# Optimization experiments

Measured on AMD Instinct MI355X. Metric: run time of the kernel, lower is better.

Reference implementation:

```python
import jax, jax.numpy as jnp
import numpy as np

# dims
B, F, K = 64, 4096, 8
D_IN = D_SLOT = D_KVQ = 192
HID = 768
N_ITERS = 3
EPS = 1e-8
GROUPS = [(0, 1), (1, 7), (7, 8)]  # bg / fg / ag contiguous slot slices
SB_STRENGTH = 1.0
SB_SIGMA = 0.25
GRID = 64  # sqrt(F)


def _layernorm(x, g, b):
    m = jnp.mean(x, axis=-1, keepdims=True)
    v = jnp.mean(jnp.square(x - m), axis=-1, keepdims=True)
    return (x - m) * jax.lax.rsqrt(v + 1e-5) * g + b


def _gru_cell(x, h, Wih, Whh, bih, bhh):
    # torch.nn.GRUCell semantics; gate order r, z, n
    gi = x @ Wih.T + bih
    gh = h @ Whh.T + bhh
    ir, iz, i_n = jnp.split(gi, 3, axis=-1)
    hr, hz, h_n = jnp.split(gh, 3, axis=-1)
    r = jax.nn.sigmoid(ir + hr)
    z = jax.nn.sigmoid(iz + hz)
    n = jnp.tanh(i_n + r * h_n)
    return (1.0 - z) * n + z * h


def _token_coords():
    y = np.linspace(-1.0, 1.0, GRID, dtype=np.float32)
    x = np.linspace(-1.0, 1.0, GRID, dtype=np.float32)
    yy, xx = np.meshgrid(y, x, indexing='ij')
    return jnp.asarray(np.stack((xx, yy), axis=-1).reshape(F, 2))


def setup_inputs() -> dict:
    key = jax.random.key(0)
    ks = jax.random.split(key, 16)
    def n(i, shape, s=0.02):
        return jax.random.normal(ks[i], shape, jnp.float32) * s
    return dict(
        features=jax.random.normal(ks[0], (B, F, D_IN), jnp.float32),
        slots=jax.random.normal(ks[1], (B, K, D_SLOT), jnp.float32),
        Wk=n(2, (D_IN, D_KVQ)), Wv=n(3, (D_IN, D_KVQ)), Wq=n(4, (D_SLOT, D_KVQ)),
        ln_feat_g=jnp.ones(D_IN), ln_feat_b=jnp.zeros(D_IN),
        ln_slot_g=jnp.ones(D_SLOT), ln_slot_b=jnp.zeros(D_SLOT),
        gru_Wih=n(5, (3, 3 * D_SLOT, D_KVQ)), gru_Whh=n(6, (3, 3 * D_SLOT, D_SLOT)),
        gru_bih=n(7, (3, 3 * D_SLOT)), gru_bhh=n(8, (3, 3 * D_SLOT)),
        mlp_ln_g=jnp.ones((3, D_SLOT)), mlp_ln_b=jnp.zeros((3, D_SLOT)),
        mlp_W1=n(9, (3, D_SLOT, HID)), mlp_b1=n(10, (3, HID)),
        mlp_W2=n(11, (3, HID, D_SLOT)), mlp_b2=n(12, (3, D_SLOT)),
    )


def reference(features, slots, Wk, Wv, Wq, ln_feat_g, ln_feat_b, ln_slot_g,
              ln_slot_b, gru_Wih, gru_Whh, gru_bih, gru_bhh, mlp_ln_g,
              mlp_ln_b, mlp_W1, mlp_b1, mlp_W2, mlp_b2):
    coords = _token_coords()  # (F, 2)
    f = _layernorm(features, ln_feat_g, ln_feat_b)
    k = f @ Wk  # (B, F, Dk)
    v = f @ Wv
    scale = D_KVQ ** -0.5
    sigma2 = max(SB_SIGMA ** 2, 1e-8)
    prev_attn = None
    for _ in range(N_ITERS):
        slots_prev = slots
        q = _layernorm(slots, ln_slot_g, ln_slot_b) @ Wq  # (B, K, Dk)
        dots = jnp.einsum('bkd,bfd->bkf', q, k) * scale
        if prev_attn is not None and SB_STRENGTH > 0.0:
            w = prev_attn / (prev_attn.sum(-1, keepdims=True) + 1e-8)
            centers = jnp.einsum('bkf,fd->bkd', w, coords)  # (B, K, 2)
            diff = coords[None, None] - centers[:, :, None]  # (B, K, F, 2)
            dist2 = jnp.sum(diff * diff, axis=-1)
            dots = dots + SB_STRENGTH * (-dist2 / (2.0 * sigma2))
        attn = jax.nn.softmax(dots, axis=1)  # competition over slots
        prev_attn = attn
        w = attn / (attn.sum(-1, keepdims=True) + EPS)  # weighted mean over F
        updates = jnp.einsum('bkf,bfd->bkd', w, v)  # (B, K, Dk)
        outs = []
        for g, (s, e) in enumerate(GROUPS):
            u = updates[:, s:e].reshape(-1, D_KVQ)
            h_prev = slots_prev[:, s:e].reshape(-1, D_SLOT)
            h = _gru_cell(u, h_prev, gru_Wih[g], gru_Whh[g], gru_bih[g], gru_bhh[g])
            x = _layernorm(h, mlp_ln_g[g], mlp_ln_b[g])
            x = jax.nn.relu(x @ mlp_W1[g] + mlp_b1[g]) @ mlp_W2[g] + mlp_b2[g]
            outs.append((h + x).reshape(B, e - s, D_SLOT))
        slots = jnp.concatenate(outs, axis=1)
    return slots
```

## Files before the change

kernel.cpp:

```cpp
#include <hip/hip_runtime.h>

typedef unsigned short u16;
typedef unsigned int u32;

#define BB 64
#define FF 4096
#define DD 192
#define HH 768

typedef __attribute__((ext_vector_type(8))) __bf16 bf16x8;
typedef __attribute__((ext_vector_type(4))) float f32x4;

__device__ __forceinline__ float bf2f(u32 u) {
  union { u32 i; float f; } x; x.i = u << 16; return x.f;
}
__device__ __forceinline__ u16 f2bf(float f) {
  __bf16 h = (__bf16)f;
  return __builtin_bit_cast(u16, h);
}
__device__ __forceinline__ u32 pk2bf(float a, float b) {
  return (u32)f2bf(a) | ((u32)f2bf(b) << 16);
}
__device__ __forceinline__ float sigm(float x) { return 1.f / (1.f + __expf(-x)); }

__global__ void prep_wmod(const float* __restrict__ Wk, const float* __restrict__ Wv,
                          const float* __restrict__ g, const float* __restrict__ bb,
                          u16* __restrict__ wmodT, float* __restrict__ s1,
                          float* __restrict__ s0) {
  int n = blockIdx.x * 64 + threadIdx.x;
  const float* W = (n < DD) ? Wk : Wv;
  int col = (n < DD) ? n : n - DD;
  float a1 = 0.f, a0 = 0.f;
  for (int e = 0; e < DD; ++e) {
    float w = W[e * DD + col];
    u16 h = f2bf(g[e] * w);
    wmodT[n * DD + e] = h;
    a1 += bf2f(h);
    a0 += bb[e] * w;
  }
  s1[n] = a1; s0[n] = a0;
}

__global__ void prep_packw(const float* __restrict__ Wih, const float* __restrict__ Whh,
                           const float* __restrict__ W1, const float* __restrict__ W2,
                           u16* __restrict__ pWih, u16* __restrict__ pWhh,
                           u16* __restrict__ pW1, u16* __restrict__ pW2) {
  int which = blockIdx.y;
  int total, N, E;
  const float* src; u16* dst; int srcEmajor;
  if (which < 2) { total = 3 * 576 * 192; N = 576; E = 192; srcEmajor = 0;
                   src = which ? Whh : Wih; dst = which ? pWhh : pWih; }
  else if (which == 2) { total = 3 * 192 * 768; N = 768; E = 192; srcEmajor = 1;
                         src = W1; dst = pW1; }
  else { total = 3 * 768 * 192; N = 192; E = 768; srcEmajor = 1; src = W2; dst = pW2; }
  for (int idx = blockIdx.x * 256 + threadIdx.x; idx < total; idx += gridDim.x * 256) {
    int g = idx / (N * E), rem = idx % (N * E);
    int n, e;
    if (srcEmajor) { e = rem / N; n = rem % N; }
    else { n = rem / E; e = rem % E; }
    dst[((g * (E / 2) + (e >> 1)) * N + n) * 2 + (e & 1)] = f2bf(src[idx]);
  }
}

__global__ __launch_bounds__(256, 4) void proj_kernel(
    const float* __restrict__ feat, const u16* __restrict__ wmodT,
    const float* __restrict__ s1, const float* __restrict__ s0,
    u16* __restrict__ kc_, u16* __restrict__ vc_) {
  __shared__ __align__(16) u16 Atile[32 * 192];
  __shared__ float stats[32 * 2];
  int tid = threadIdx.x;
  long tile_base = (long)blockIdx.x * 32;
  int w = tid >> 6, lane = tid & 63;
  {
    int r = w * 8 + (lane >> 3);
    int p = lane & 7;
    const float4* src = (const float4*)(feat + (tile_base + r) * DD) + p * 6;
    float s = 0.f, s2 = 0.f;
    #pragma unroll
    for (int i = 0; i < 6; ++i) {
      float4 v = src[i];
      s += v.x + v.y + v.z + v.w;
      s2 += v.x * v.x + v.y * v.y + v.z * v.z + v.w * v.w;
      uint2 pk;
      pk.x = pk2bf(v.x, v.y);
      pk.y = pk2bf(v.z, v.w);
      int u = p * 3 + (i >> 1);
      *(uint2*)((char*)Atile + r * 384 + ((u ^ (r & 7)) << 4) + (i & 1) * 8) = pk;
    }
    s += __shfl_xor(s, 1); s2 += __shfl_xor(s2, 1);
    s += __shfl_xor(s, 2); s2 += __shfl_xor(s2, 2);
    s += __shfl_xor(s, 4); s2 += __shfl_xor(s2, 4);
    if (p == 0) {
      float mu = s * (1.f / 192.f);
      stats[r * 2] = mu;
      stats[r * 2 + 1] = rsqrtf(s2 * (1.f / 192.f) - mu * mu + 1e-5f);
    }
  }
  __syncthreads();
  int l15 = lane & 15, l4 = lane >> 4;
  f32x4 acc[2][6];
  #pragma unroll
  for (int a = 0; a < 2; ++a)
    #pragma unroll
    for (int b2 = 0; b2 < 6; ++b2) acc[a][b2] = (f32x4){0.f, 0.f, 0.f, 0.f};
  #pragma unroll
  for (int kk = 0; kk < 6; ++kk) {
    bf16x8 afr[2];
    #pragma unroll
    for (int mt = 0; mt < 2; ++mt) {
      int row = mt * 16 + l15;
      int u = kk * 4 + l4;
      afr[mt] = *(bf16x8*)((char*)Atile + row * 384 + ((u ^ (row & 7)) << 4));
    }
    bf16x8 bfr[6];
    #pragma unroll
    for (int nt = 0; nt < 6; ++nt) {
      int col = w * 96 + nt * 16 + l15;
      bfr[nt] = *(const bf16x8*)(wmodT + col * DD + kk * 32 + l4 * 8);
    }
    #pragma unroll
    for (int mt = 0; mt < 2; ++mt)
      #pragma unroll
      for (int nt = 0; nt < 6; ++nt)
        acc[mt][nt] = __builtin_amdgcn_mfma_f32_16x16x32_bf16(afr[mt], bfr[nt],
                                                              acc[mt][nt], 0, 0, 0);
  }
  __syncthreads();
  long bidx = tile_base / FF;
  int f0 = (int)(tile_base % FF);
  if (w < 2) {
    #pragma unroll
    for (int nt = 0; nt < 6; ++nt) {
      int col = w * 96 + nt * 16 + l15;
      float s1c = s1[col], s0c = s0[col];
      int u = col >> 3, ce = (col & 7) * 2;
      #pragma unroll
      for (int mt = 0; mt < 2; ++mt) {
        #pragma unroll
        for (int j = 0; j < 4; ++j) {
          int row = mt * 16 + l4 * 4 + j;
          float mu = stats[row * 2], rstd = stats[row * 2 + 1];
          u16 hv = f2bf(rstd * (acc[mt][nt][j] - mu * s1c) + s0c);
          *(u16*)((char*)Atile + row * 384 + ((u ^ (row & 7)) << 4) + ce) = hv;
        }
      }
    }
  } else {
    #pragma unroll
    for (int nt = 0; nt < 6; ++nt) {
      int col = (w - 2) * 96 + nt * 16 + l15;
      float s1c = s1[col + 192], s0c = s0[col + 192];
      int ntg = col >> 4;
      #pragma unroll
      for (int mt = 0; mt < 2; ++mt) {
        int tl = mt * 16 + l4 * 4;
        int r0 = tl, r1 = tl + 1, r2 = tl + 2, r3 = tl + 3;
        uint2 pk;
        pk.x = pk2bf(stats[r0 * 2 + 1] * (acc[mt][nt][0] - stats[r0 * 2] * s1c) + s0c,
                     stats[r1 * 2 + 1] * (acc[mt][nt][1] - stats[r1 * 2] * s1c) + s0c);
        pk.y = pk2bf(stats[r2 * 2 + 1] * (acc[mt][nt][2] - stats[r2 * 2] * s1c) + s0c,
                     stats[r3 * 2 + 1] * (acc[mt][nt][3] - stats[r3 * 2] * s1c) + s0c);
        u32 ox = __shfl_xor((int)pk.x, 16);
        u32 oy = __shfl_xor((int)pk.y, 16);
        if ((l4 & 1) == 0) {
          int t0 = f0 + tl;
          int g32 = t0 >> 5;
          int l4f = (t0 >> 3) & 3;
          uint4 val = {pk.x, pk.y, ox, oy};
          *(uint4*)(vc_ + ((((long)bidx * 128 + g32) * 12 + ntg) * 64 + l4f * 16 +
                           (col & 15)) * 8) = val;
        }
      }
    }
  }
  __syncthreads();
  {
    long Tg0 = tile_base >> 4;
    #pragma unroll
    for (int p2 = 0; p2 < 3; ++p2) {
      int fi = tid + p2 * 256;
      int tau = fi & 15, u = (fi >> 4) % 24, tt = fi / 384;
      uint4 val = *(uint4*)((char*)Atile + (tt * 16 + tau) * 384 + ((u ^ (tau & 7)) << 4));
      *(uint4*)(kc_ + (((Tg0 + tt) * 24 + u) * 16 + tau) * 8) = val;
    }
  }
}

__global__ __launch_bounds__(64) void qproj_kernel(
    const float* __restrict__ slots, const float* __restrict__ Wq,
    const float* __restrict__ g, const float* __restrict__ bb,
    float* __restrict__ qbuf) {
  __shared__ float ln[192];
  int bk = blockIdx.x;
  int lane = threadIdx.x;
  const float* x = slots + bk * DD;
  float v0 = x[lane], v1 = x[lane + 64], v2 = x[lane + 128];
  float s = v0 + v1 + v2, s2 = v0 * v0 + v1 * v1 + v2 * v2;
  #pragma unroll
  for (int m = 1; m < 64; m <<= 1) { s += __shfl_xor(s, m); s2 += __shfl_xor(s2, m); }
  float mu = s * (1.f / 192.f);
  float rstd = rsqrtf(s2 * (1.f / 192.f) - mu * mu + 1e-5f);
  ln[lane]       = (v0 - mu) * rstd * g[lane]       + bb[lane];
  ln[lane + 64]  = (v1 - mu) * rstd * g[lane + 64]  + bb[lane + 64];
  ln[lane + 128] = (v2 - mu) * rstd * g[lane + 128] + bb[lane + 128];
  __syncthreads();
  float a0 = 0.f, a1 = 0.f, a2 = 0.f;
  for (int e = 0; e < DD; ++e) {
    float le = ln[e];
    a0 += le * Wq[e * DD + lane];
    a1 += le * Wq[e * DD + lane + 64];
    a2 += le * Wq[e * DD + lane + 128];
  }
  const float scale = 0.07216878364870323f;
  qbuf[bk * DD + lane]       = a0 * scale;
  qbuf[bk * DD + lane + 64]  = a1 * scale;
  qbuf[bk * DD + lane + 128] = a2 * scale;
}

__global__ __launch_bounds__(256) void attnupd_kernel(
    const u16* __restrict__ kc_, const u16* __restrict__ vc_,
    const float* __restrict__ qbuf,
    const float* __restrict__ asum_prev, const float* __restrict__ cacc_prev,
    float* __restrict__ upd, float* __restrict__ asum_cur,
    float* __restrict__ cacc_cur, int have_bias) {
  __shared__ __align__(16) u16 qlds[16 * 192];
  __shared__ __align__(16) u16 attn_lds[16 * 256];
  int b = blockIdx.x;
  int chunk = blockIdx.y * 256;
  int tid = threadIdx.x;
  if (tid < 192) {
    int s = tid / 24, u = tid % 24;
    const float* qp = qbuf + (b * 8 + s) * DD + u * 8;
    uint4 p;
    p.x = pk2bf(qp[0], qp[1]);
    p.y = pk2bf(qp[2], qp[3]);
    p.z = pk2bf(qp[4], qp[5]);
    p.w = pk2bf(qp[6], qp[7]);
    *(uint4*)((char*)qlds + s * 384 + ((u ^ (s & 7)) << 4)) = p;
  } else {
    int t2 = tid - 192;
    #pragma unroll
    for (int i = 0; i < 3; ++i) {
      int idx = t2 * 3 + i;
      int s = 8 + idx / 24, u = idx % 24;
      *(uint4*)((char*)qlds + s * 384 + ((u ^ (s & 7)) << 4)) = (uint4){0, 0, 0, 0};
    }
    #pragma unroll
    for (int i = 0; i < 4; ++i)
      *(uint4*)((char*)attn_lds + 4096 + (t2 * 4 + i) * 16) = (uint4){0, 0, 0, 0};
  }
  __syncthreads();
  int w = tid >> 6, lane = tid & 63;
  int l15 = lane & 15, l4 = lane >> 4;
  bf16x8 qfr[6];
  #pragma unroll
  for (int kk = 0; kk < 6; ++kk) {
    int u = kk * 4 + l4;
    qfr[kk] = *(bf16x8*)((char*)qlds + l15 * 384 + ((u ^ (l15 & 7)) << 4));
  }
  float ax[4], ay[4], c0[4];
  #pragma unroll
  for (int j = 0; j < 4; ++j) {
    int s = l4 * 4 + j;
    if (have_bias && s < 8) {
      float inv = 1.f / (asum_prev[b * 8 + s] + 1e-8f);
      float cx = cacc_prev[(b * 8 + s) * 2] * inv;
      float cy = cacc_prev[(b * 8 + s) * 2 + 1] * inv;
      ax[j] = 16.f * cx; ay[j] = 16.f * cy; c0[j] = -8.f * (cx * cx + cy * cy);
    } else { ax[j] = 0.f; ay[j] = 0.f; c0[j] = 0.f; }
  }
  float pa[4], px[4], py[4];
  #pragma unroll
  for (int j = 0; j < 4; ++j) { pa[j] = 0.f; px[j] = 0.f; py[j] = 0.f; }
  for (int tile = w; tile < 16; tile += 4) {
    int t0 = chunk + tile * 16;
    long Tg = (long)b * 256 + (t0 >> 4);
    const u16* kp = kc_ + (Tg * 24 + l4) * 128 + l15 * 8;
    f32x4 acc = (f32x4){0.f, 0.f, 0.f, 0.f};
    #pragma unroll
    for (int kk = 0; kk < 6; ++kk) {
      bf16x8 bfr = *(const bf16x8*)(kp + kk * 512);
      acc = __builtin_amdgcn_mfma_f32_16x16x32_bf16(qfr[kk], bfr, acc, 0, 0, 0);
    }
    int t = t0 + l15;
    float x = -1.f + (float)(t & 63) * (2.f / 63.f);
    float y = -1.f + (float)(t >> 6) * (2.f / 63.f);
    float m8r2 = -8.f * (x * x + y * y);
    float d4[4];
    #pragma unroll
    for (int j = 0; j < 4; ++j)
      d4[j] = acc[j] + (have_bias ? (ax[j] * x + ay[j] * y + c0[j] + m8r2) : 0.f);
    float o4[4];
    #pragma unroll
    for (int j = 0; j < 4; ++j) o4[j] = __shfl_xor(d4[j], 16);
    float mx = fmaxf(fmaxf(fmaxf(d4[0], d4[1]), fmaxf(d4[2], d4[3])),
                     fmaxf(fmaxf(o4[0], o4[1]), fmaxf(o4[2], o4[3])));
    float e4[4];
    float sum = 0.f;
    #pragma unroll
    for (int j = 0; j < 4; ++j) { e4[j] = __expf(d4[j] - mx); sum += e4[j]; }
    #pragma unroll
    for (int j = 0; j < 4; ++j) sum += __expf(o4[j] - mx);
    float inv = 1.f / sum;
    if (l4 < 2) {
      int tl = tile * 16 + l15;
      #pragma unroll
      for (int j = 0; j < 4; ++j) {
        float a = e4[j] * inv;
        int s = l4 * 4 + j;
        *(u16*)((char*)attn_lds + ((s * 512 + tl * 2) ^ ((s & 7) << 4))) = f2bf(a);
        pa[j] += a; px[j] += a * x; py[j] += a * y;
      }
    }
  }
  #pragma unroll
  for (int m = 1; m < 16; m <<= 1) {
    #pragma unroll
    for (int j = 0; j < 4; ++j) {
      pa[j] += __shfl_xor(pa[j], m);
      px[j] += __shfl_xor(px[j], m);
      py[j] += __shfl_xor(py[j], m);
    }
  }
  if (l15 == 0 && l4 < 2) {
    #pragma unroll
    for (int j = 0; j < 4; ++j) {
      int s = l4 * 4 + j;
      atomicAdd(&asum_cur[b * 8 + s], pa[j]);
      atomicAdd(&cacc_cur[(b * 8 + s) * 2], px[j]);
      atomicAdd(&cacc_cur[(b * 8 + s) * 2 + 1], py[j]);
    }
  }
  __syncthreads();
  int g32base = chunk >> 5;
  #pragma unroll
  for (int ni = 0; ni < 3; ++ni) {
    int nt = w * 3 + ni;
    f32x4 acc = (f32x4){0.f, 0.f, 0.f, 0.f};
    const u16* vp = vc_ + ((((long)b * 128 + g32base) * 12 + nt) * 64 + l4 * 16 + l15) * 8;
    #pragma unroll
    for (int gl = 0; gl < 8; ++gl) {
      int tl0 = gl * 32 + l4 * 8;
      bf16x8 afr = *(bf16x8*)((char*)attn_lds + ((l15 * 512 + tl0 * 2) ^ ((l15 & 7) << 4)));
      bf16x8 bfr = *(const bf16x8*)(vp + gl * 12 * 64 * 8);
      acc = __builtin_amdgcn_mfma_f32_16x16x32_bf16(afr, bfr, acc, 0, 0, 0);
    }
    if (l4 < 2) {
      #pragma unroll
      for (int j = 0; j < 4; ++j) {
        int s = l4 * 4 + j;
        atomicAdd(&upd[((long)b * 8 + s) * DD + nt * 16 + l15], acc[j]);
      }
    }
  }
}

template <int M>
__device__ void gru_body(int b0, int g, int srow,
                         float* u_l, float* h_l, float* gi_l, float* gh_l,
                         float* hn_l, float* ln_l, float* x1_l, float* out_l, float* st,
                         const float* __restrict__ upd, const float* __restrict__ asum,
                         const float* __restrict__ sin_,
                         const u16* __restrict__ pWih, const u16* __restrict__ pWhh,
                         const float* __restrict__ bih, const float* __restrict__ bhh,
                         const float* __restrict__ mlng, const float* __restrict__ mlnb,
                         const u16* __restrict__ pW1, const float* __restrict__ b1,
                         const u16* __restrict__ pW2, const float* __restrict__ b2,
                         float* __restrict__ sout) {
  int tid = threadIdx.x;
  for (int idx = tid; idx < M * 192; idx += 768) {
    int row = idx / 192, d = idx % 192;
    int gr = b0 * 8 + srow + row;
    float inv = 1.f / (asum[gr] + 1e-8f);
    u_l[row * 192 + d] = upd[gr * DD + d] * inv;
    h_l[row * 192 + d] = sin_[gr * DD + d];
  }
  __syncthreads();
  if (tid < 576) {
    int c = tid;
    const u16* wih = pWih + (size_t)g * 96 * 1152 + c * 2;
    const u16* whh = pWhh + (size_t)g * 96 * 1152 + c * 2;
    float ai[M], ah[M];
    #pragma unroll
    for (int r = 0; r < M; ++r) { ai[r] = 0.f; ah[r] = 0.f; }
    #pragma unroll 4
    for (int e2 = 0; e2 < 96; ++e2) {
      u32 wi = *(const u32*)(wih + e2 * 1152);
      u32 wh = *(const u32*)(whh + e2 * 1152);
      float wi0 = bf2f(wi & 0xffffu), wi1 = bf2f(wi >> 16);
      float wh0 = bf2f(wh & 0xffffu), wh1 = bf2f(wh >> 16);
      #pragma unroll
      for (int r = 0; r < M; ++r) {
        ai[r] += wi0 * u_l[r * 192 + e2 * 2] + wi1 * u_l[r * 192 + e2 * 2 + 1];
        ah[r] += wh0 * h_l[r * 192 + e2 * 2] + wh1 * h_l[r * 192 + e2 * 2 + 1];
      }
    }
    #pragma unroll
    for (int r = 0; r < M; ++r) { gi_l[r * 576 + c] = ai[r]; gh_l[r * 576 + c] = ah[r]; }
  }
  __syncthreads();
  if (tid < M * 192) {
    int row = tid / 192, uu = tid % 192;
    const float* bihg = bih + g * 576;
    const float* bhhg = bhh + g * 576;
    float r_ = sigm(gi_l[row * 576 + uu] + bihg[uu] + gh_l[row * 576 + uu] + bhhg[uu]);
    float z_ = sigm(gi_l[row * 576 + 192 + uu] + bihg[192 + uu] +
                    gh_l[row * 576 + 192 + uu] + bhhg[192 + uu]);
    float nn = gi_l[row * 576 + 384 + uu] + bihg[384 + uu] +
               r_ * (gh_l[row * 576 + 384 + uu] + bhhg[384 + uu]);
    float t = 1.f - 2.f / (__expf(2.f * nn) + 1.f);
    hn_l[row * 192 + uu] = (1.f - z_) * t + z_ * h_l[row * 192 + uu];
  }
  __syncthreads();
  {
    int wv = tid >> 6, lane = tid & 63;
    if (wv < M) {
      float v0 = hn_l[wv * 192 + lane], v1 = hn_l[wv * 192 + lane + 64],
            v2 = hn_l[wv * 192 + lane + 128];
      float s = v0 + v1 + v2, sq = v0 * v0 + v1 * v1 + v2 * v2;
      #pragma unroll
      for (int m = 1; m < 64; m <<= 1) { s += __shfl_xor(s, m); sq += __shfl_xor(sq, m); }
      if (lane == 0) {
        float mu = s * (1.f / 192.f);
        st[wv * 2] = mu;
        st[wv * 2 + 1] = rsqrtf(sq * (1.f / 192.f) - mu * mu + 1e-5f);
      }
    }
  }
  __syncthreads();
  if (tid < M * 192) {
    int row = tid / 192, uu = tid % 192;
    ln_l[row * 192 + uu] = (hn_l[row * 192 + uu] - st[row * 2]) * st[row * 2 + 1] *
                               mlng[g * DD + uu] + mlnb[g * DD + uu];
  }
  __syncthreads();
  {
    int c = tid;
    const u16* w1 = pW1 + (size_t)g * 96 * 1536 + c * 2;
    float a[M];
    #pragma unroll
    for (int r = 0; r < M; ++r) a[r] = 0.f;
    #pragma unroll 4
    for (int e2 = 0; e2 < 96; ++e2) {
      u32 wp = *(const u32*)(w1 + e2 * 1536);
      float w0 = bf2f(wp & 0xffffu), w1f = bf2f(wp >> 16);
      #pragma unroll
      for (int r = 0; r < M; ++r)
        a[r] += w0 * ln_l[r * 192 + e2 * 2] + w1f * ln_l[r * 192 + e2 * 2 + 1];
    }
    float bc = b1[g * HH + c];
    #pragma unroll
    for (int r = 0; r < M; ++r) x1_l[r * 768 + c] = fmaxf(a[r] + bc, 0.f);
  }
  if (tid < M * 192) {
    int row = tid / 192, uu = tid % 192;
    out_l[row * 192 + uu] = hn_l[row * 192 + uu] + b2[g * DD + uu];
  }
  __syncthreads();
  {
    int c = tid % 192, ks = tid / 192;
    const u16* w2 = pW2 + (size_t)g * 384 * 384 + c * 2;
    float a[M];
    #pragma unroll
    for (int r = 0; r < M; ++r) a[r] = 0.f;
    #pragma unroll 4
    for (int e2 = ks * 96; e2 < ks * 96 + 96; ++e2) {
      u32 wp = *(const u32*)(w2 + e2 * 384);
      float w0 = bf2f(wp & 0xffffu), w1f = bf2f(wp >> 16);
      #pragma unroll
      for (int r = 0; r < M; ++r)
        a[r] += w0 * x1_l[r * 768 + e2 * 2] + w1f * x1_l[r * 768 + e2 * 2 + 1];
    }
    #pragma unroll
    for (int r = 0; r < M; ++r) atomicAdd(&out_l[r * 192 + c], a[r]);
  }
  __syncthreads();
  if (tid < M * 192) {
    int row = tid / 192, d = tid % 192;
    sout[(b0 * 8 + srow + row) * DD + d] = out_l[row * 192 + d];
  }
}

__global__ __launch_bounds__(768) void gru_kernel(
    const float* __restrict__ upd, const float* __restrict__ asum,
    const float* __restrict__ sin_,
    const u16* __restrict__ pWih, const u16* __restrict__ pWhh,
    const float* __restrict__ bih, const float* __restrict__ bhh,
    const float* __restrict__ mlng, const float* __restrict__ mlnb,
    const u16* __restrict__ pW1, const float* __restrict__ b1,
    const u16* __restrict__ pW2, const float* __restrict__ b2,
    float* __restrict__ sout) {
  __shared__ float u_l[3 * 192], h_l[3 * 192], gi_l[3 * 576], gh_l[3 * 576];
  __shared__ float hn_l[3 * 192], ln_l[3 * 192], x1_l[3 * 768], out_l[3 * 192], st[8];
  int b = blockIdx.x, y = blockIdx.y;
  if (y == 0)
    gru_body<1>(b, 0, 0, u_l, h_l, gi_l, gh_l, hn_l, ln_l, x1_l, out_l, st,
                upd, asum, sin_, pWih, pWhh, bih, bhh, mlng, mlnb, pW1, b1, pW2, b2, sout);
  else if (y == 1)
    gru_body<1>(b, 2, 7, u_l, h_l, gi_l, gh_l, hn_l, ln_l, x1_l, out_l, st,
                upd, asum, sin_, pWih, pWhh, bih, bhh, mlng, mlnb, pW1, b1, pW2, b2, sout);
  else if (y == 2)
    gru_body<3>(b, 1, 1, u_l, h_l, gi_l, gh_l, hn_l, ln_l, x1_l, out_l, st,
                upd, asum, sin_, pWih, pWhh, bih, bhh, mlng, mlnb, pW1, b1, pW2, b2, sout);
  else
    gru_body<3>(b, 1, 4, u_l, h_l, gi_l, gh_l, hn_l, ln_l, x1_l, out_l, st,
                upd, asum, sin_, pWih, pWhh, bih, bhh, mlng, mlnb, pW1, b1, pW2, b2, sout);
}

extern "C" void kernel_launch(void* const* d_in, const int* in_sizes, int n_in,
                              void* d_out, int out_size, void* d_ws, size_t ws_size,
                              hipStream_t stream) {
  const float* feat = (const float*)d_in[0];
  const float* slots = (const float*)d_in[1];
  const float* Wk = (const float*)d_in[2];
  const float* Wv = (const float*)d_in[3];
  const float* Wq = (const float*)d_in[4];
  const float* lfg = (const float*)d_in[5];
  const float* lfb = (const float*)d_in[6];
  const float* lsg = (const float*)d_in[7];
  const float* lsb = (const float*)d_in[8];
  const float* gWih = (const float*)d_in[9];
  const float* gWhh = (const float*)d_in[10];
  const float* gbih = (const float*)d_in[11];
  const float* gbhh = (const float*)d_in[12];
  const float* mlng = (const float*)d_in[13];
  const float* mlnb = (const float*)d_in[14];
  const float* W1 = (const float*)d_in[15];
  const float* b1 = (const float*)d_in[16];
  const float* W2 = (const float*)d_in[17];
  const float* b2 = (const float*)d_in[18];
  float* out = (float*)d_out;

  char* ws = (char*)d_ws;
  size_t off = 0;
  auto alloc = [&](size_t bytes) {
    void* p = ws + off;
    off += (bytes + 255) & ~(size_t)255;
    return p;
  };
  u16* kc_    = (u16*)alloc((size_t)BB * FF * DD * 2);
  u16* vc_    = (u16*)alloc((size_t)BB * DD * FF * 2);
  float* qbuf = (float*)alloc((size_t)BB * 8 * DD * 4);
  float* upd  = (float*)alloc((size_t)BB * 8 * DD * 4);
  float* slA  = (float*)alloc((size_t)BB * 8 * DD * 4);
  float* slB  = (float*)alloc((size_t)BB * 8 * DD * 4);
  float* asum0 = (float*)alloc(BB * 8 * 4);
  float* asum1 = (float*)alloc(BB * 8 * 4);
  float* cacc0 = (float*)alloc(BB * 8 * 2 * 4);
  float* cacc1 = (float*)alloc(BB * 8 * 2 * 4);
  u16* wmodT  = (u16*)alloc(384 * DD * 2);
  float* s1   = (float*)alloc(384 * 4);
  float* s0   = (float*)alloc(384 * 4);
  u16* pWih   = (u16*)alloc((size_t)3 * 576 * DD * 2);
  u16* pWhh   = (u16*)alloc((size_t)3 * 576 * DD * 2);
  u16* pW1    = (u16*)alloc((size_t)3 * DD * HH * 2);
  u16* pW2    = (u16*)alloc((size_t)3 * HH * DD * 2);

  prep_wmod<<<6, 64, 0, stream>>>(Wk, Wv, lfg, lfb, wmodT, s1, s0);
  prep_packw<<<dim3(432, 4), 256, 0, stream>>>(gWih, gWhh, W1, W2, pWih, pWhh, pW1, pW2);
  proj_kernel<<<BB * FF / 32, 256, 0, stream>>>(feat, wmodT, s1, s0, kc_, vc_);

  const float* sin_ = slots;
  float* souts[3] = {slA, slB, out};
  float* asums[2] = {asum0, asum1};
  float* caccs[2] = {cacc0, cacc1};
  for (int it = 0; it < 3; ++it) {
    int cur = it & 1, prev = cur ^ 1;
    hipMemsetAsync(upd, 0, BB * 8 * DD * 4, stream);
    hipMemsetAsync(asums[cur], 0, BB * 8 * 4, stream);
    hipMemsetAsync(caccs[cur], 0, BB * 8 * 2 * 4, stream);
    qproj_kernel<<<BB * 8, 64, 0, stream>>>(sin_, Wq, lsg, lsb, qbuf);
    attnupd_kernel<<<dim3(BB, 16), 256, 0, stream>>>(kc_, vc_, qbuf, asums[prev],
                                                     caccs[prev], upd, asums[cur],
                                                     caccs[cur], it > 0 ? 1 : 0);
    gru_kernel<<<dim3(BB, 4), 768, 0, stream>>>(upd, asums[cur], sin_, pWih, pWhh,
                                                gbih, gbhh, mlng, mlnb, pW1, b1, pW2, b2,
                                                souts[it]);
    sin_ = souts[it];
  }
}
```

Before: 490.4 us.

## Restructure projection to per-wave 16-token tiles and fold memsets into qproj

The projection kernel now gives each wave its own 16-token tile. Each wave loads features straight into registers as MFMA A-fragments and computes the LayerNorm stats with shuffles, which removes the shared A-tile staging and block-wide barriers. Each wave loops over the four 96-column output groups and stages K output through a private LDS buffer, so the grid is half as many blocks holding twice the tokens. The three hipMemsetAsync calls per iteration are folded into the qproj kernel, which saves launches. The trade-off is that each wave re-reads the full weight matrix from global/L2, and the 4-group loop is serialized.

```diff
diff --git a/kernel.cpp b/kernel.cpp
--- a/kernel.cpp
+++ b/kernel.cpp
@@ -64,106 +64,97 @@
 
 __global__ __launch_bounds__(256, 4) void proj_kernel(
     const float* __restrict__ feat, const u16* __restrict__ wmodT,
-    const float* __restrict__ s1, const float* __restrict__ s0,
+    const float* __restrict__ s1v, const float* __restrict__ s0v,
     u16* __restrict__ kc_, u16* __restrict__ vc_) {
-  __shared__ __align__(16) u16 Atile[32 * 192];
-  __shared__ float stats[32 * 2];
+  __shared__ __align__(16) u16 Ctile[4][2176];
   int tid = threadIdx.x;
-  long tile_base = (long)blockIdx.x * 32;
   int w = tid >> 6, lane = tid & 63;
-  {
-    int r = w * 8 + (lane >> 3);
-    int p = lane & 7;
-    const float4* src = (const float4*)(feat + (tile_base + r) * DD) + p * 6;
-    float s = 0.f, s2 = 0.f;
-    #pragma unroll
-    for (int i = 0; i < 6; ++i) {
-      float4 v = src[i];
-      s += v.x + v.y + v.z + v.w;
-      s2 += v.x * v.x + v.y * v.y + v.z * v.z + v.w * v.w;
-      uint2 pk;
-      pk.x = pk2bf(v.x, v.y);
-      pk.y = pk2bf(v.z, v.w);
-      int u = p * 3 + (i >> 1);
-      *(uint2*)((char*)Atile + r * 384 + ((u ^ (r & 7)) << 4) + (i & 1) * 8) = pk;
-    }
-    s += __shfl_xor(s, 1); s2 += __shfl_xor(s2, 1);
-    s += __shfl_xor(s, 2); s2 += __shfl_xor(s2, 2);
-    s += __shfl_xor(s, 4); s2 += __shfl_xor(s2, 4);
-    if (p == 0) {
-      float mu = s * (1.f / 192.f);
-      stats[r * 2] = mu;
-      stats[r * 2 + 1] = rsqrtf(s2 * (1.f / 192.f) - mu * mu + 1e-5f);
-    }
-  }
-  __syncthreads();
   int l15 = lane & 15, l4 = lane >> 4;
-  f32x4 acc[2][6];
-  #pragma unroll
-  for (int a = 0; a < 2; ++a)
-    #pragma unroll
-    for (int b2 = 0; b2 < 6; ++b2) acc[a][b2] = (f32x4){0.f, 0.f, 0.f, 0.f};
+  long wtile = (long)blockIdx.x * 4 + w;
+  long tok0 = wtile * 16;
+  int bidx = (int)(wtile >> 8);
+  int f0 = ((int)wtile & 255) * 16;
+  char* ct = (char*)&Ctile[w][0];
+
+  const float* fp = feat + (tok0 + l15) * DD + l4 * 8;
+  float4 xa[6], xb[6];
   #pragma unroll
   for (int kk = 0; kk < 6; ++kk) {
-    bf16x8 afr[2];
-    #pragma unroll
-    for (int mt = 0; mt < 2; ++mt) {
-      int row = mt * 16 + l15;
-      int u = kk * 4 + l4;
-      afr[mt] = *(bf16x8*)((char*)Atile + row * 384 + ((u ^ (row & 7)) << 4));
-    }
-    bf16x8 bfr[6];
-    #pragma unroll
-    for (int nt = 0; nt < 6; ++nt) {
-      int col = w * 96 + nt * 16 + l15;
-      bfr[nt] = *(const bf16x8*)(wmodT + col * DD + kk * 32 + l4 * 8);
-    }
-    #pragma unroll
-    for (int mt = 0; mt < 2; ++mt)
-      #pragma unroll
-      for (int nt = 0; nt < 6; ++nt)
-        acc[mt][nt] = __builtin_amdgcn_mfma_f32_16x16x32_bf16(afr[mt], bfr[nt],
-                                                              acc[mt][nt], 0, 0, 0);
-  }
-  __syncthreads();
-  long bidx = tile_base / FF;
-  int f0 = (int)(tile_base % FF);
-  if (w < 2) {
-    #pragma unroll
-    for (int nt = 0; nt < 6; ++nt) {
-      int col = w * 96 + nt * 16 + l15;
-      float s1c = s1[col], s0c = s0[col];
-      int u = col >> 3, ce = (col & 7) * 2;
-      #pragma unroll
-      for (int mt = 0; mt < 2; ++mt) {
+    xa[kk] = *(const float4*)(fp + kk * 32);
+    xb[kk] = *(const float4*)(fp + kk * 32 + 4);
+  }
+  float s = 0.f, s2 = 0.f;
+  bf16x8 afr[6];
+  #pragma unroll
+  for (int kk = 0; kk < 6; ++kk) {
+    float4 a = xa[kk], b = xb[kk];
+    s += a.x + a.y + a.z + a.w + b.x + b.y + b.z + b.w;
+    s2 += a.x * a.x + a.y * a.y + a.z * a.z + a.w * a.w +
+          b.x * b.x + b.y * b.y + b.z * b.z + b.w * b.w;
+    union { u32 u[4]; bf16x8 v; } cv;
+    cv.u[0] = pk2bf(a.x, a.y); cv.u[1] = pk2bf(a.z, a.w);
+    cv.u[2] = pk2bf(b.x, b.y); cv.u[3] = pk2bf(b.z, b.w);
+    afr[kk] = cv.v;
+  }
+  s += __shfl_xor(s, 16); s2 += __shfl_xor(s2, 16);
+  s += __shfl_xor(s, 32); s2 += __shfl_xor(s2, 32);
+  float mu = s * (1.f / 192.f);
+  float rstd = rsqrtf(s2 * (1.f / 192.f) - mu * mu + 1e-5f);
+  float muv[4], rsv[4];
+  #pragma unroll
+  for (int j = 0; j < 4; ++j) {
+    muv[j] = __shfl(mu, l4 * 4 + j);
+    rsv[j] = __shfl(rstd, l4 * 4 + j);
+  }
+
+  #pragma unroll 1
+  for (int grp = 0; grp < 4; ++grp) {
+    f32x4 acc[6];
+    #pragma unroll
+    for (int nt = 0; nt < 6; ++nt) acc[nt] = (f32x4){0.f, 0.f, 0.f, 0.f};
+    #pragma unroll
+    for (int kk = 0; kk < 6; ++kk) {
+      #pragma unroll
+      for (int nt = 0; nt < 6; ++nt) {
+        int col = grp * 96 + nt * 16 + l15;
+        bf16x8 bfr = *(const bf16x8*)(wmodT + col * DD + kk * 32 + l4 * 8);
+        acc[nt] = __builtin_amdgcn_mfma_f32_16x16x32_bf16(afr[kk], bfr, acc[nt], 0, 0, 0);
+      }
+    }
+    if (grp < 2) {
+      #pragma unroll
+      for (int nt = 0; nt < 6; ++nt) {
+        int col = nt * 16 + l15;
+        float s1c = s1v[grp * 96 + col], s0c = s0v[grp * 96 + col];
         #pragma unroll
         for (int j = 0; j < 4; ++j) {
-          int row = mt * 16 + l4 * 4 + j;
-          float mu = stats[row * 2], rstd = stats[row * 2 + 1];
-          u16 hv = f2bf(rstd * (acc[mt][nt][j] - mu * s1c) + s0c);
-          *(u16*)((char*)Atile + row * 384 + ((u ^ (row & 7)) << 4) + ce) = hv;
+          int tau = l4 * 4 + j;
+          u16 hv = f2bf(rsv[j] * (acc[nt][j] - muv[j] * s1c) + s0c);
+          *(u16*)(ct + tau * 272 + (col >> 3) * 16 + (col & 7) * 2) = hv;
         }
       }
-    }
-  } else {
-    #pragma unroll
-    for (int nt = 0; nt < 6; ++nt) {
-      int col = (w - 2) * 96 + nt * 16 + l15;
-      float s1c = s1[col + 192], s0c = s0[col + 192];
-      int ntg = col >> 4;
-      #pragma unroll
-      for (int mt = 0; mt < 2; ++mt) {
-        int tl = mt * 16 + l4 * 4;
-        int r0 = tl, r1 = tl + 1, r2 = tl + 2, r3 = tl + 3;
+      #pragma unroll
+      for (int it = 0; it < 3; ++it) {
+        int fi = lane + it * 64;
+        int g = fi >> 4, tau = fi & 15;
+        uint4 val = *(uint4*)(ct + tau * 272 + g * 16);
+        *(uint4*)(kc_ + (((long)wtile * 24 + grp * 12 + g) * 16 + tau) * 8) = val;
+      }
+    } else {
+      #pragma unroll
+      for (int nt = 0; nt < 6; ++nt) {
+        int col = (grp - 2) * 96 + nt * 16 + l15;
+        float s1c = s1v[col + 192], s0c = s0v[col + 192];
+        int ntg = col >> 4;
         uint2 pk;
-        pk.x = pk2bf(stats[r0 * 2 + 1] * (acc[mt][nt][0] - stats[r0 * 2] * s1c) + s0c,
-                     stats[r1 * 2 + 1] * (acc[mt][nt][1] - stats[r1 * 2] * s1c) + s0c);
-        pk.y = pk2bf(stats[r2 * 2 + 1] * (acc[mt][nt][2] - stats[r2 * 2] * s1c) + s0c,
-                     stats[r3 * 2 + 1] * (acc[mt][nt][3] - stats[r3 * 2] * s1c) + s0c);
+        pk.x = pk2bf(rsv[0] * (acc[nt][0] - muv[0] * s1c) + s0c,
+                     rsv[1] * (acc[nt][1] - muv[1] * s1c) + s0c);
+        pk.y = pk2bf(rsv[2] * (acc[nt][2] - muv[2] * s1c) + s0c,
+                     rsv[3] * (acc[nt][3] - muv[3] * s1c) + s0c);
         u32 ox = __shfl_xor((int)pk.x, 16);
         u32 oy = __shfl_xor((int)pk.y, 16);
         if ((l4 & 1) == 0) {
-          int t0 = f0 + tl;
+          int t0 = f0 + l4 * 4;
           int g32 = t0 >> 5;
           int l4f = (t0 >> 3) & 3;
           uint4 val = {pk.x, pk.y, ox, oy};
@@ -173,26 +164,23 @@
       }
     }
   }
-  __syncthreads();
-  {
-    long Tg0 = tile_base >> 4;
-    #pragma unroll
-    for (int p2 = 0; p2 < 3; ++p2) {
-      int fi = tid + p2 * 256;
-      int tau = fi & 15, u = (fi >> 4) % 24, tt = fi / 384;
-      uint4 val = *(uint4*)((char*)Atile + (tt * 16 + tau) * 384 + ((u ^ (tau & 7)) << 4));
-      *(uint4*)(kc_ + (((Tg0 + tt) * 24 + u) * 16 + tau) * 8) = val;
-    }
-  }
 }
 
 __global__ __launch_bounds__(64) void qproj_kernel(
     const float* __restrict__ slots, const float* __restrict__ Wq,
     const float* __restrict__ g, const float* __restrict__ bb,
-    float* __restrict__ qbuf) {
+    float* __restrict__ qbuf, float* __restrict__ upd,
+    float* __restrict__ asum_cur, float* __restrict__ cacc_cur) {
   __shared__ float ln[192];
   int bk = blockIdx.x;
   int lane = threadIdx.x;
+  {
+    int gtid = bk * 64 + lane;
+    float4 z = {0.f, 0.f, 0.f, 0.f};
+    if (gtid < 24576) ((float4*)upd)[gtid] = z;
+    else if (gtid < 24576 + 128) ((float4*)asum_cur)[gtid - 24576] = z;
+    else if (gtid < 24576 + 384) ((float4*)cacc_cur)[gtid - 24704] = z;
+  }
   const float* x = slots + bk * DD;
   float v0 = x[lane], v1 = x[lane + 64], v2 = x[lane + 128];
   float s = v0 + v1 + v2, s2 = v0 * v0 + v1 * v1 + v2 * v2;
@@ -558,7 +546,7 @@
 
   prep_wmod<<<6, 64, 0, stream>>>(Wk, Wv, lfg, lfb, wmodT, s1, s0);
   prep_packw<<<dim3(432, 4), 256, 0, stream>>>(gWih, gWhh, W1, W2, pWih, pWhh, pW1, pW2);
-  proj_kernel<<<BB * FF / 32, 256, 0, stream>>>(feat, wmodT, s1, s0, kc_, vc_);
+  proj_kernel<<<BB * FF / 64, 256, 0, stream>>>(feat, wmodT, s1, s0, kc_, vc_);
 
   const float* sin_ = slots;
   float* souts[3] = {slA, slB, out};
@@ -566,10 +554,8 @@
   float* caccs[2] = {cacc0, cacc1};
   for (int it = 0; it < 3; ++it) {
     int cur = it & 1, prev = cur ^ 1;
-    hipMemsetAsync(upd, 0, BB * 8 * DD * 4, stream);
-    hipMemsetAsync(asums[cur], 0, BB * 8 * 4, stream);
-    hipMemsetAsync(caccs[cur], 0, BB * 8 * 2 * 4, stream);
-    qproj_kernel<<<BB * 8, 64, 0, stream>>>(sin_, Wq, lsg, lsb, qbuf);
+    qproj_kernel<<<BB * 8, 64, 0, stream>>>(sin_, Wq, lsg, lsb, qbuf,
+                                            upd, asums[cur], caccs[cur]);
     attnupd_kernel<<<dim3(BB, 16), 256, 0, stream>>>(kc_, vc_, qbuf, asums[prev],
                                                      caccs[prev], upd, asums[cur],
                                                      caccs[cur], it > 0 ? 1 : 0);
```

Result: slower. 593.4 us (+21.0%).

## Make projection kernel persistent with prefetch and fold memsets into qproj

Applied to the files above, without the earlier changes.

The projection kernel now processes four 32-row tiles per block (2048 blocks), prefetching the next tile's features into registers while the current tile runs its MFMA work. K output is staged in a separate padded per-wave Ctile so waves 0-1 can write it out without an extra block-wide barrier. The three per-iteration hipMemsetAsync calls are replaced by zeroing inside qproj_kernel, which removes launch overhead. In exchange the kernel uses more registers and shared memory, and launches fewer blocks.

```diff
diff --git a/kernel.cpp b/kernel.cpp
--- a/kernel.cpp
+++ b/kernel.cpp
@@ -64,124 +64,139 @@
 
 __global__ __launch_bounds__(256, 4) void proj_kernel(
     const float* __restrict__ feat, const u16* __restrict__ wmodT,
-    const float* __restrict__ s1, const float* __restrict__ s0,
+    const float* __restrict__ s1v, const float* __restrict__ s0v,
     u16* __restrict__ kc_, u16* __restrict__ vc_) {
   __shared__ __align__(16) u16 Atile[32 * 192];
-  __shared__ float stats[32 * 2];
+  __shared__ __align__(16) char Ctile[2][32 * 208];
+  __shared__ float stats[64];
   int tid = threadIdx.x;
-  long tile_base = (long)blockIdx.x * 32;
   int w = tid >> 6, lane = tid & 63;
+  int l15 = lane & 15, l4 = lane >> 4;
+  int r = w * 8 + (lane >> 3), p = lane & 7;
+  long T0 = (long)blockIdx.x * 4;
+
+  float4 cur[6], nxt[6];
   {
-    int r = w * 8 + (lane >> 3);
-    int p = lane & 7;
-    const float4* src = (const float4*)(feat + (tile_base + r) * DD) + p * 6;
-    float s = 0.f, s2 = 0.f;
-    #pragma unroll
-    for (int i = 0; i < 6; ++i) {
-      float4 v = src[i];
-      s += v.x + v.y + v.z + v.w;
-      s2 += v.x * v.x + v.y * v.y + v.z * v.z + v.w * v.w;
-      uint2 pk;
-      pk.x = pk2bf(v.x, v.y);
-      pk.y = pk2bf(v.z, v.w);
-      int u = p * 3 + (i >> 1);
-      *(uint2*)((char*)Atile + r * 384 + ((u ^ (r & 7)) << 4) + (i & 1) * 8) = pk;
-    }
-    s += __shfl_xor(s, 1); s2 += __shfl_xor(s2, 1);
-    s += __shfl_xor(s, 2); s2 += __shfl_xor(s2, 2);
-    s += __shfl_xor(s, 4); s2 += __shfl_xor(s2, 4);
-    if (p == 0) {
-      float mu = s * (1.f / 192.f);
-      stats[r * 2] = mu;
-      stats[r * 2 + 1] = rsqrtf(s2 * (1.f / 192.f) - mu * mu + 1e-5f);
-    }
-  }
-  __syncthreads();
-  int l15 = lane & 15, l4 = lane >> 4;
-  f32x4 acc[2][6];
+    const float4* src = (const float4*)(feat + (T0 * 32 + r) * DD);
+    #pragma unroll
+    for (int i = 0; i < 6; ++i) cur[i] = src[i * 8 + p];
+  }
+
   #pragma unroll
-  for (int a = 0; a < 2; ++a)
-    #pragma unroll
-    for (int b2 = 0; b2 < 6; ++b2) acc[a][b2] = (f32x4){0.f, 0.f, 0.f, 0.f};
-  #pragma unroll
-  for (int kk = 0; kk < 6; ++kk) {
-    bf16x8 afr[2];
-    #pragma unroll
-    for (int mt = 0; mt < 2; ++mt) {
-      int row = mt * 16 + l15;
-      int u = kk * 4 + l4;
-      afr[mt] = *(bf16x8*)((char*)Atile + row * 384 + ((u ^ (row & 7)) << 4));
-    }
-    bf16x8 bfr[6];
-    #pragma unroll
-    for (int nt = 0; nt < 6; ++nt) {
-      int col = w * 96 + nt * 16 + l15;
-      bfr[nt] = *(const bf16x8*)(wmodT + col * DD + kk * 32 + l4 * 8);
-    }
-    #pragma unroll
-    for (int mt = 0; mt < 2; ++mt)
-      #pragma unroll
-      for (int nt = 0; nt < 6; ++nt)
-        acc[mt][nt] = __builtin_amdgcn_mfma_f32_16x16x32_bf16(afr[mt], bfr[nt],
-                                                              acc[mt][nt], 0, 0, 0);
-  }
-  __syncthreads();
-  long bidx = tile_base / FF;
-  int f0 = (int)(tile_base % FF);
-  if (w < 2) {
-    #pragma unroll
-    for (int nt = 0; nt < 6; ++nt) {
-      int col = w * 96 + nt * 16 + l15;
-      float s1c = s1[col], s0c = s0[col];
-      int u = col >> 3, ce = (col & 7) * 2;
+  for (int t = 0; t < 4; ++t) {
+    long T = T0 + t;
+    {
+      float s = 0.f, s2 = 0.f;
+      #pragma unroll
+      for (int i = 0; i < 6; ++i) {
+        float4 v = cur[i];
+        s += v.x + v.y + v.z + v.w;
+        s2 += v.x * v.x + v.y * v.y + v.z * v.z + v.w * v.w;
+        int fidx = i * 8 + p;
+        int u = fidx >> 1, half = fidx & 1;
+        uint2 pk;
+        pk.x = pk2bf(v.x, v.y);
+        pk.y = pk2bf(v.z, v.w);
+        *(uint2*)((char*)Atile + r * 384 + ((u ^ (r & 7)) << 4) + half * 8) = pk;
+      }
+      s += __shfl_xor(s, 1); s2 += __shfl_xor(s2, 1);
+      s += __shfl_xor(s, 2); s2 += __shfl_xor(s2, 2);
+      s += __shfl_xor(s, 4); s2 += __shfl_xor(s2, 4);
+      if (p == 0) {
+        float mu = s * (1.f / 192.f);
+        stats[r * 2] = mu;
+        stats[r * 2 + 1] = rsqrtf(s2 * (1.f / 192.f) - mu * mu + 1e-5f);
+      }
+    }
+    __syncthreads();
+    if (t < 3) {
+      const float4* src = (const float4*)(feat + ((T + 1) * 32 + r) * DD);
+      #pragma unroll
+      for (int i = 0; i < 6; ++i) nxt[i] = src[i * 8 + p];
+    }
+    f32x4 acc[2][6];
+    #pragma unroll
+    for (int a = 0; a < 2; ++a)
+      #pragma unroll
+      for (int b2 = 0; b2 < 6; ++b2) acc[a][b2] = (f32x4){0.f, 0.f, 0.f, 0.f};
+    #pragma unroll
+    for (int kk = 0; kk < 6; ++kk) {
+      bf16x8 afr[2];
       #pragma unroll
       for (int mt = 0; mt < 2; ++mt) {
+        int row = mt * 16 + l15;
+        int u = kk * 4 + l4;
+        afr[mt] = *(bf16x8*)((char*)Atile + row * 384 + ((u ^ (row & 7)) << 4));
+      }
+      #pragma unroll
+      for (int nt = 0; nt < 6; ++nt) {
+        int col = w * 96 + nt * 16 + l15;
+        bf16x8 bfr = *(const bf16x8*)(wmodT + col * DD + kk * 32 + l4 * 8);
         #pragma unroll
-        for (int j = 0; j < 4; ++j) {
-          int row = mt * 16 + l4 * 4 + j;
-          float mu = stats[row * 2], rstd = stats[row * 2 + 1];
-          u16 hv = f2bf(rstd * (acc[mt][nt][j] - mu * s1c) + s0c);
-          *(u16*)((char*)Atile + row * 384 + ((u ^ (row & 7)) << 4) + ce) = hv;
+        for (int mt = 0; mt < 2; ++mt)
+          acc[mt][nt] = __builtin_amdgcn_mfma_f32_16x16x32_bf16(afr[mt], bfr,
+                                                                acc[mt][nt], 0, 0, 0);
+      }
+    }
+    int bidx = (int)(T >> 7);
+    int f0 = ((int)T & 127) * 32;
+    if (w < 2) {
+      char* ct = Ctile[w];
+      #pragma unroll
+      for (int nt = 0; nt < 6; ++nt) {
+        int c = nt * 16 + l15;
+        float s1c = s1v[w * 96 + c], s0c = s0v[w * 96 + c];
+        #pragma unroll
+        for (int mt = 0; mt < 2; ++mt) {
+          #pragma unroll
+          for (int j = 0; j < 4; ++j) {
+            int row = mt * 16 + l4 * 4 + j;
+            float mu = stats[row * 2], rstd = stats[row * 2 + 1];
+            u16 hv = f2bf(rstd * (acc[mt][nt][j] - mu * s1c) + s0c);
+            *(u16*)(ct + row * 208 + ((c >> 3) << 4) + (c & 7) * 2) = hv;
+          }
         }
       }
-    }
-  } else {
-    #pragma unroll
-    for (int nt = 0; nt < 6; ++nt) {
-      int col = (w - 2) * 96 + nt * 16 + l15;
-      float s1c = s1[col + 192], s0c = s0[col + 192];
-      int ntg = col >> 4;
-      #pragma unroll
-      for (int mt = 0; mt < 2; ++mt) {
-        int tl = mt * 16 + l4 * 4;
-        int r0 = tl, r1 = tl + 1, r2 = tl + 2, r3 = tl + 3;
-        uint2 pk;
-        pk.x = pk2bf(stats[r0 * 2 + 1] * (acc[mt][nt][0] - stats[r0 * 2] * s1c) + s0c,
-                     stats[r1 * 2 + 1] * (acc[mt][nt][1] - stats[r1 * 2] * s1c) + s0c);
-        pk.y = pk2bf(stats[r2 * 2 + 1] * (acc[mt][nt][2] - stats[r2 * 2] * s1c) + s0c,
-                     stats[r3 * 2 + 1] * (acc[mt][nt][3] - stats[r3 * 2] * s1c) + s0c);
-        u32 ox = __shfl_xor((int)pk.x, 16);
-        u32 oy = __shfl_xor((int)pk.y, 16);
-        if ((l4 & 1) == 0) {
-          int t0 = f0 + tl;
-          int g32 = t0 >> 5;
-          int l4f = (t0 >> 3) & 3;
-          uint4 val = {pk.x, pk.y, ox, oy};
-          *(uint4*)(vc_ + ((((long)bidx * 128 + g32) * 12 + ntg) * 64 + l4f * 16 +
-                           (col & 15)) * 8) = val;
+      asm volatile("s_waitcnt lgkmcnt(0)" ::: "memory");
+      #pragma unroll
+      for (int it = 0; it < 6; ++it) {
+        int fi = it * 64 + lane;
+        int tau = fi & 15, g = (fi >> 4) % 12, tt = fi / 192;
+        uint4 val = *(uint4*)(ct + (tt * 16 + tau) * 208 + g * 16);
+        *(uint4*)(kc_ + ((T * 2 + tt) * 24 + w * 12 + g) * 128 + tau * 8) = val;
+      }
+    } else {
+      #pragma unroll
+      for (int nt = 0; nt < 6; ++nt) {
+        int col = (w - 2) * 96 + nt * 16 + l15;
+        float s1c = s1v[col + 192], s0c = s0v[col + 192];
+        int ntg = col >> 4;
+        #pragma unroll
+        for (int mt = 0; mt < 2; ++mt) {
+          int tl = mt * 16 + l4 * 4;
+          int r0 = tl, r1 = tl + 1, r2 = tl + 2, r3 = tl + 3;
+          uint2 pk;
+          pk.x = pk2bf(stats[r0 * 2 + 1] * (acc[mt][nt][0] - stats[r0 * 2] * s1c) + s0c,
+                       stats[r1 * 2 + 1] * (acc[mt][nt][1] - stats[r1 * 2] * s1c) + s0c);
+          pk.y = pk2bf(stats[r2 * 2 + 1] * (acc[mt][nt][2] - stats[r2 * 2] * s1c) + s0c,
+                       stats[r3 * 2 + 1] * (acc[mt][nt][3] - stats[r3 * 2] * s1c) + s0c);
+          u32 ox = __shfl_xor((int)pk.x, 16);
+          u32 oy = __shfl_xor((int)pk.y, 16);
+          if ((l4 & 1) == 0) {
+            int t0 = f0 + tl;
+            int g32 = t0 >> 5;
+            int l4f = (t0 >> 3) & 3;
+            uint4 val = {pk.x, pk.y, ox, oy};
+            *(uint4*)(vc_ + ((((long)bidx * 128 + g32) * 12 + ntg) * 64 + l4f * 16 +
+                             (col & 15)) * 8) = val;
+          }
         }
       }
     }
-  }
-  __syncthreads();
-  {
-    long Tg0 = tile_base >> 4;
-    #pragma unroll
-    for (int p2 = 0; p2 < 3; ++p2) {
-      int fi = tid + p2 * 256;
-      int tau = fi & 15, u = (fi >> 4) % 24, tt = fi / 384;
-      uint4 val = *(uint4*)((char*)Atile + (tt * 16 + tau) * 384 + ((u ^ (tau & 7)) << 4));
-      *(uint4*)(kc_ + (((Tg0 + tt) * 24 + u) * 16 + tau) * 8) = val;
+    __syncthreads();
+    if (t < 3) {
+      #pragma unroll
+      for (int i = 0; i < 6; ++i) cur[i] = nxt[i];
     }
   }
 }
@@ -189,10 +204,18 @@
 __global__ __launch_bounds__(64) void qproj_kernel(
     const float* __restrict__ slots, const float* __restrict__ Wq,
     const float* __restrict__ g, const float* __restrict__ bb,
-    float* __restrict__ qbuf) {
+    float* __restrict__ qbuf, float* __restrict__ upd,
+    float* __restrict__ asum_cur, float* __restrict__ cacc_cur) {
   __shared__ float ln[192];
   int bk = blockIdx.x;
   int lane = threadIdx.x;
+  {
+    int gtid = bk * 64 + lane;
+    float4 z = {0.f, 0.f, 0.f, 0.f};
+    if (gtid < 24576) ((float4*)upd)[gtid] = z;
+    else if (gtid < 24576 + 128) ((float4*)asum_cur)[gtid - 24576] = z;
+    else if (gtid < 24576 + 384) ((float4*)cacc_cur)[gtid - 24704] = z;
+  }
   const float* x = slots + bk * DD;
   float v0 = x[lane], v1 = x[lane + 64], v2 = x[lane + 128];
   float s = v0 + v1 + v2, s2 = v0 * v0 + v1 * v1 + v2 * v2;
@@ -558,7 +581,7 @@
 
   prep_wmod<<<6, 64, 0, stream>>>(Wk, Wv, lfg, lfb, wmodT, s1, s0);
   prep_packw<<<dim3(432, 4), 256, 0, stream>>>(gWih, gWhh, W1, W2, pWih, pWhh, pW1, pW2);
-  proj_kernel<<<BB * FF / 32, 256, 0, stream>>>(feat, wmodT, s1, s0, kc_, vc_);
+  proj_kernel<<<2048, 256, 0, stream>>>(feat, wmodT, s1, s0, kc_, vc_);
 
   const float* sin_ = slots;
   float* souts[3] = {slA, slB, out};
@@ -566,10 +589,8 @@
   float* caccs[2] = {cacc0, cacc1};
   for (int it = 0; it < 3; ++it) {
     int cur = it & 1, prev = cur ^ 1;
-    hipMemsetAsync(upd, 0, BB * 8 * DD * 4, stream);
-    hipMemsetAsync(asums[cur], 0, BB * 8 * 4, stream);
-    hipMemsetAsync(caccs[cur], 0, BB * 8 * 2 * 4, stream);
-    qproj_kernel<<<BB * 8, 64, 0, stream>>>(sin_, Wq, lsg, lsb, qbuf);
+    qproj_kernel<<<BB * 8, 64, 0, stream>>>(sin_, Wq, lsg, lsb, qbuf,
+                                            upd, asums[cur], caccs[cur]);
     attnupd_kernel<<<dim3(BB, 16), 256, 0, stream>>>(kc_, vc_, qbuf, asums[prev],
                                                      caccs[prev], upd, asums[cur],
                                                      caccs[cur], it > 0 ? 1 : 0);
```

Result: slower. 606.2 us (+23.6%).
